# Optimization experiments

Measured on AMD Instinct MI355X. Metric: run time of the kernel, lower is better.

The kernel has to match this reference:

```python
import jax, jax.numpy as jnp
import numpy as np

H = W = M = 16          # 3D token grid
N = H * W * M           # 4096 tokens
D = 256                 # dims == out_dim == key/value dim == x1_dim
HC = 8                  # head_count
D2 = 2 * D              # concat width
C2 = 4 * D              # MixFFN hidden
OUT = D                 # out_dim
UP = OUT // 2           # PatchExpand output channels
B = 4


def _ln(x, g, b, eps=1e-5):
    m = jnp.mean(x, axis=-1, keepdims=True)
    v = jnp.mean(jnp.square(x - m), axis=-1, keepdims=True)
    return (x - m) / jnp.sqrt(v + eps) * g + b


def setup_inputs() -> dict:
    key = jax.random.key(0)
    ks = jax.random.split(key, 16)
    s = 0.02
    inp = {
        "x1": jax.random.normal(ks[0], (B, N, D), jnp.float32),
        "x2": jax.random.normal(ks[1], (B, N, D), jnp.float32),
        # x1_linear (x1_dim -> out_dim)
        "w_x1": s * jax.random.normal(ks[2], (D, OUT), jnp.float32),
        "b_x1": jnp.zeros((OUT,), jnp.float32),
        # CrossAttentionBlock.norm1 (shared for x1 and x2)
        "g_n1": jnp.ones((D,), jnp.float32),
        "be_n1": jnp.zeros((D,), jnp.float32),
        # Cross_Attention.reprojection: 1x1x1 Conv3d D -> 2D == channel matmul
        "w_rep": s * jax.random.normal(ks[3], (D, D2), jnp.float32),
        "b_rep": jnp.zeros((D2,), jnp.float32),
        # Cross_Attention.norm (LayerNorm 2D)
        "g_an": jnp.ones((D2,), jnp.float32),
        "be_an": jnp.zeros((D2,), jnp.float32),
        # CrossAttentionBlock.norm2 (LayerNorm 2D)
        "g_n2": jnp.ones((D2,), jnp.float32),
        "be_n2": jnp.zeros((D2,), jnp.float32),
        # MixFFN_skip fc1 (2D -> 4D), depthwise conv3d, norm1, fc2
        "w_fc1": s * jax.random.normal(ks[4], (D2, C2), jnp.float32),
        "b_fc1": jnp.zeros((C2,), jnp.float32),
        "w_dw": s * jax.random.normal(ks[5], (C2, 1, 3, 3, 3), jnp.float32),
        "b_dw": jnp.zeros((C2,), jnp.float32),
        "g_m1": jnp.ones((C2,), jnp.float32),
        "be_m1": jnp.zeros((C2,), jnp.float32),
        "w_fc2": s * jax.random.normal(ks[6], (C2, D2), jnp.float32),
        "b_fc2": jnp.zeros((D2,), jnp.float32),
        # concat_linear (2*dims -> out_dim)
        "w_cat": s * jax.random.normal(ks[7], (D2, OUT), jnp.float32),
        "b_cat": jnp.zeros((OUT,), jnp.float32),
        # PatchExpand: expand (out_dim -> 4*out_dim, no bias) + LayerNorm(out_dim//2)
        "w_exp": s * jax.random.normal(ks[8], (OUT, 4 * OUT), jnp.float32),
        "g_up": jnp.ones((UP,), jnp.float32),
        "be_up": jnp.zeros((UP,), jnp.float32),
    }
    return inp


def reference(x1, x2, w_x1, b_x1, g_n1, be_n1, w_rep, b_rep, g_an, be_an,
              g_n2, be_n2, w_fc1, b_fc1, w_dw, b_dw, g_m1, be_m1,
              w_fc2, b_fc2, w_cat, b_cat, w_exp, g_up, be_up):
    b = x1.shape[0]
    hk = D // HC  # head key channels (== head value channels here)

    # x1_linear
    x1e = x1 @ w_x1 + b_x1                                 # [B,N,D]

    # shared norm1 applied to both streams
    n1 = _ln(x1e, g_n1, be_n1)
    n2 = _ln(x2, g_n1, be_n1)

    # Cross_Attention (efficient attention, softmax-normalized K/Q)
    kq = jnp.transpose(n2, (0, 2, 1)).reshape(b, HC, hk, N)   # keys==queries
    val = jnp.transpose(n1, (0, 2, 1)).reshape(b, HC, hk, N)
    k = jax.nn.softmax(kq, axis=3)          # softmax over tokens
    q = jax.nn.softmax(kq, axis=2)          # softmax over head channels
    ctx = jnp.einsum('bhkn,bhvn->bhkv', k, val)        # [B,HC,hk,hv]
    att = jnp.einsum('bhkv,bhkn->bhvn', ctx, q)        # [B,HC,hv,N]
    att = att.reshape(b, D, N)                          # concat heads
    # 1x1x1 Conv3d reprojection D -> 2D, then to [B,N,2D] + LayerNorm
    rep = jnp.einsum('bdn,de->bne', att, w_rep) + b_rep
    rep = _ln(rep, g_an, be_an)                         # [B,N,2D]

    # residual concat + attention
    tx = jnp.concatenate([x1e, x2], axis=2) + rep       # [B,N,2D]

    # MixFFN_skip
    h = _ln(tx, g_n2, be_n2) @ w_fc1 + b_fc1            # [B,N,C2]
    hv = jnp.transpose(h, (0, 2, 1)).reshape(b, C2, H, W, M)
    dw = jax.lax.conv_general_dilated(
        hv, w_dw, window_strides=(1, 1, 1), padding='SAME',
        feature_group_count=C2,
        dimension_numbers=('NCDHW', 'OIDHW', 'NCDHW'))
    dw = dw + b_dw[None, :, None, None, None]
    dw = jnp.transpose(dw.reshape(b, C2, N), (0, 2, 1))  # [B,N,C2]
    ax = jax.nn.gelu(_ln(dw + h, g_m1, be_m1), approximate=False)
    mx = tx + (ax @ w_fc2 + b_fc2)                       # [B,N,2D]

    # concat_linear
    y = mx @ w_cat + b_cat                               # [B,N,OUT]

    ye = y @ w_exp                                       # [B,N,4*OUT]
    ye = ye.reshape(b, 8 * N, UP)                        # view+reshape of contiguous
    out = _ln(ye, g_up, be_up)                           # [B,8N,OUT//2]
    return out
```

## Files before the change

### kernel.cpp

```cpp
#include <hip/hip_runtime.h>
#include <math.h>

using u16 = unsigned short;
typedef __bf16 bf16x8 __attribute__((ext_vector_type(8)));
typedef _Float16 h16x8 __attribute__((ext_vector_type(8)));
typedef _Float16 h2 __attribute__((ext_vector_type(2)));
typedef float f32x4 __attribute__((ext_vector_type(4)));

#define BB 4
#define NN 4096
#define DD 256
#define DD2 512
#define CC2 1024
static constexpr int ROWS = BB * NN;
static constexpr size_t MB = 1024 * 1024;

__device__ __forceinline__ u16 f2bf(float f) {
  union { float f; unsigned u; } v; v.f = f;
  unsigned r = v.u + 0x7fffu + ((v.u >> 16) & 1u);
  return (u16)(r >> 16);
}
__device__ __forceinline__ float bf2f(u16 u) {
  union { unsigned u; float f; } v; v.u = ((unsigned)u) << 16;
  return v.f;
}
__device__ __forceinline__ u16 f2h(float f) {
  union { _Float16 h; u16 u; } v; v.h = (_Float16)f; return v.u;
}
__device__ __forceinline__ void gload16(const void* g, void* l) {
  __builtin_amdgcn_global_load_lds(
      (const __attribute__((address_space(1))) void*)g,
      (__attribute__((address_space(3))) void*)l, 16, 0, 0);
}

__global__ __launch_bounds__(256) void wprep_all(
    const float* __restrict__ w_x1, const float* __restrict__ w_rep,
    const float* __restrict__ w_fc1, const float* __restrict__ w_fc2,
    const float* __restrict__ w_cat, const float* __restrict__ w_exp,
    const float* __restrict__ w_dw,
    u16* __restrict__ w_x1t, u16* __restrict__ w_rept,
    u16* __restrict__ w_fc1t, u16* __restrict__ w_fc2h,
    u16* __restrict__ w_catt, u16* __restrict__ w_expt,
    unsigned* __restrict__ w_dwh) {
  int i = blockIdx.x * 256 + threadIdx.x;
  if (i < 65536) { int n = i >> 8, k = i & 255; w_x1t[i] = f2bf(w_x1[k * 256 + n]); return; }
  i -= 65536;
  if (i < 131072) { int n = i >> 8, k = i & 255; w_rept[i] = f2bf(w_rep[k * 512 + n]); return; }
  i -= 131072;
  if (i < 524288) { int n = i >> 9, k = i & 511; w_fc1t[i] = f2bf(w_fc1[k * 1024 + n]); return; }
  i -= 524288;
  if (i < 524288) { int n = i >> 10, k = i & 1023; w_fc2h[i] = f2h(w_fc2[k * 512 + n]); return; }
  i -= 524288;
  if (i < 131072) { int n = i >> 9, k = i & 511; w_catt[i] = f2bf(w_cat[k * 256 + n]); return; }
  i -= 131072;
  if (i < 262144) { int n = i >> 8, k = i & 255; w_expt[i] = f2bf(w_exp[k * 1024 + n]); return; }
  i -= 262144;
  if (i < 13824) {
    int tap = i >> 9, cp = i & 511;
    unsigned lo = f2h(w_dw[(2 * cp) * 27 + tap]);
    unsigned hi = f2h(w_dw[(2 * cp + 1) * 27 + tap]);
    w_dwh[i] = lo | (hi << 16);
  }
}

template <int K, int EPI, bool AF32 = false, bool PERB = false, bool F16 = false>
__global__ __launch_bounds__(256, 2) void gemm_mfma(
    const u16* __restrict__ A, const u16* __restrict__ Bt,
    const float* __restrict__ bias, const u16* __restrict__ resid,
    void* __restrict__ Cout, int nTilesN,
    const float* __restrict__ gup, const float* __restrict__ beup) {
  const int t = threadIdx.x;
  const int bid = blockIdx.x;
  const int m0 = (bid / nTilesN) * 128;
  const int n0 = (bid % nTilesN) * 128;
  const int Ncols = nTilesN * 128;
  if (PERB) Bt += (size_t)(m0 >> 12) * (size_t)Ncols * K;
  const int lane = t & 63, wid = t >> 6;
  const int wr = wid >> 1, wc = wid & 1;
  const int lrow = lane & 15, kgrp = lane >> 4;

  __shared__ u16 ldsA[2][128 * 32];
  __shared__ u16 ldsB[2][128 * 32];

  int srow[2], sslot[2];
#pragma unroll
  for (int c = 0; c < 2; ++c) {
    int idx = c * 256 + t;
    srow[c] = idx >> 2;
    sslot[c] = (idx & 3) ^ ((srow[c] >> 1) & 3);
  }

  int offA[4], offB[4];
#pragma unroll
  for (int m = 0; m < 4; ++m) {
    int r = wr * 64 + m * 16 + lrow;
    offA[m] = r * 32 + ((kgrp ^ ((r >> 1) & 3)) * 8);
  }
#pragma unroll
  for (int n = 0; n < 4; ++n) {
    int r = wc * 64 + n * 16 + lrow;
    offB[n] = r * 32 + ((kgrp ^ ((r >> 1) & 3)) * 8);
  }

  f32x4 acc[4][4];
#pragma unroll
  for (int m = 0; m < 4; ++m)
#pragma unroll
    for (int n = 0; n < 4; ++n) acc[m][n] = f32x4{0.f, 0.f, 0.f, 0.f};

  auto loadA32 = [&](int c, int kc) -> uint4 {
    const float* A32 = (const float*)A;
    const float* p = A32 + (size_t)(m0 + srow[c]) * K + kc + sslot[c] * 8;
    float4 f0 = *(const float4*)p;
    float4 f1 = *(const float4*)(p + 4);
    u16 o[8] = {f2bf(f0.x), f2bf(f0.y), f2bf(f0.z), f2bf(f0.w),
                f2bf(f1.x), f2bf(f1.y), f2bf(f1.z), f2bf(f1.w)};
    return *(uint4*)o;
  };
  auto stage_async = [&](int buf, int kc) {
#pragma unroll
    for (int c = 0; c < 2; ++c) {
      gload16(A + (size_t)(m0 + srow[c]) * K + kc + sslot[c] * 8,
              &ldsA[buf][(c * 256 + t) * 8]);
      gload16(Bt + (size_t)(n0 + srow[c]) * K + kc + sslot[c] * 8,
              &ldsB[buf][(c * 256 + t) * 8]);
    }
  };

  uint4 ra[2], rb[2];
  if constexpr (AF32) {
#pragma unroll
    for (int c = 0; c < 2; ++c) {
      ra[c] = loadA32(c, 0);
      rb[c] = *(const uint4*)(Bt + (size_t)(n0 + srow[c]) * K + sslot[c] * 8);
    }
#pragma unroll
    for (int c = 0; c < 2; ++c) {
      int idx = c * 256 + t;
      *(uint4*)&ldsA[0][idx * 8] = ra[c];
      *(uint4*)&ldsB[0][idx * 8] = rb[c];
    }
  } else {
    stage_async(0, 0);
  }
  __syncthreads();

  const int nt = K / 32;
  for (int tt = 0; tt < nt; ++tt) {
    const int cur = tt & 1;
    if (tt + 1 < nt) {
      const int kc = (tt + 1) * 32;
      if constexpr (AF32) {
#pragma unroll
        for (int c = 0; c < 2; ++c) {
          ra[c] = loadA32(c, kc);
          rb[c] = *(const uint4*)(Bt + (size_t)(n0 + srow[c]) * K + kc + sslot[c] * 8);
        }
      } else {
        stage_async(cur ^ 1, kc);
      }
    }
    if constexpr (F16) {
      h16x8 af[4], bf[4];
#pragma unroll
      for (int m = 0; m < 4; ++m) af[m] = *(const h16x8*)&ldsA[cur][offA[m]];
#pragma unroll
      for (int n = 0; n < 4; ++n) bf[n] = *(const h16x8*)&ldsB[cur][offB[n]];
#pragma unroll
      for (int m = 0; m < 4; ++m)
#pragma unroll
        for (int n = 0; n < 4; ++n)
          acc[m][n] = __builtin_amdgcn_mfma_f32_16x16x32_f16(af[m], bf[n], acc[m][n], 0, 0, 0);
    } else {
      bf16x8 af[4], bf[4];
#pragma unroll
      for (int m = 0; m < 4; ++m) af[m] = *(const bf16x8*)&ldsA[cur][offA[m]];
#pragma unroll
      for (int n = 0; n < 4; ++n) bf[n] = *(const bf16x8*)&ldsB[cur][offB[n]];
#pragma unroll
      for (int m = 0; m < 4; ++m)
#pragma unroll
        for (int n = 0; n < 4; ++n)
          acc[m][n] = __builtin_amdgcn_mfma_f32_16x16x32_bf16(af[m], bf[n], acc[m][n], 0, 0, 0);
    }
    if (AF32 && tt + 1 < nt) {
#pragma unroll
      for (int c = 0; c < 2; ++c) {
        int idx = c * 256 + t;
        *(uint4*)&ldsA[cur ^ 1][idx * 8] = ra[c];
        *(uint4*)&ldsB[cur ^ 1][idx * 8] = rb[c];
      }
    }
    __syncthreads();
  }

  if (EPI == 3) {
    __shared__ float lnS[2][128], lnQ[2][128];
    float s_[4][4], q_[4][4];
#pragma unroll
    for (int m = 0; m < 4; ++m)
#pragma unroll
      for (int j = 0; j < 4; ++j) {
        float s = 0.f, q = 0.f;
#pragma unroll
        for (int n = 0; n < 4; ++n) {
          float v = acc[m][n][j];
          s += v; q += v * v;
        }
        s_[m][j] = s; q_[m][j] = q;
      }
#pragma unroll
    for (int msk = 1; msk < 16; msk <<= 1) {
#pragma unroll
      for (int m = 0; m < 4; ++m)
#pragma unroll
        for (int j = 0; j < 4; ++j) {
          s_[m][j] += __shfl_xor(s_[m][j], msk, 64);
          q_[m][j] += __shfl_xor(q_[m][j], msk, 64);
        }
    }
    if (lrow == 0) {
#pragma unroll
      for (int m = 0; m < 4; ++m)
#pragma unroll
        for (int j = 0; j < 4; ++j) {
          int r = wr * 64 + m * 16 + kgrp * 4 + j;
          lnS[wc][r] = s_[m][j];
          lnQ[wc][r] = q_[m][j];
        }
    }
    __syncthreads();
#pragma unroll
    for (int m = 0; m < 4; ++m) {
      const int rb0 = wr * 64 + m * 16 + kgrp * 4;
#pragma unroll
      for (int j = 0; j < 4; ++j) {
        const int r = rb0 + j;
        float S = lnS[0][r] + lnS[1][r];
        float Q = lnQ[0][r] + lnQ[1][r];
        float mean = S * (1.0f / 128.0f);
        float var = Q * (1.0f / 128.0f) - mean * mean;
        float iv = rsqrtf(var + 1e-5f);
#pragma unroll
        for (int n = 0; n < 4; ++n) {
          int lc = wc * 64 + n * 16 + lrow;
          ((float*)Cout)[(size_t)(m0 + r) * Ncols + n0 + lc] =
              (acc[m][n][j] - mean) * iv * gup[lc] + beup[lc];
        }
      }
    }
    return;
  }

  float bcol[4];
#pragma unroll
  for (int n = 0; n < 4; ++n) {
    int col = n0 + wc * 64 + n * 16 + (lane & 15);
    bcol[n] = bias ? bias[col] : 0.f;
  }
#pragma unroll
  for (int m = 0; m < 4; ++m) {
    const int r0 = m0 + wr * 64 + m * 16 + kgrp * 4;
#pragma unroll
    for (int n = 0; n < 4; ++n) {
      const int col = n0 + wc * 64 + n * 16 + (lane & 15);
#pragma unroll
      for (int j = 0; j < 4; ++j) {
        float v = acc[m][n][j] + bcol[n];
        size_t idx = (size_t)(r0 + j) * Ncols + col;
        if (EPI == 0) {
          ((float*)Cout)[idx] = v;
        } else if (EPI == 1) {
          ((u16*)Cout)[idx] = f2bf(v);
        } else if (EPI == 4) {
          ((u16*)Cout)[idx] = f2h(v);
        } else {
          v += bf2f(resid[idx]);
          ((u16*)Cout)[idx] = f2bf(v);
        }
      }
    }
  }
}

__global__ __launch_bounds__(256) void ln256_both(
    const u16* __restrict__ x1e_b, const float* __restrict__ x2,
    const float* __restrict__ g, const float* __restrict__ be,
    u16* __restrict__ n1T, u16* __restrict__ n2T, u16* __restrict__ qmat) {
  int row = blockIdx.x;
  const int t = threadIdx.x;
  const bool first = row < ROWS;
  if (!first) row -= ROWS;
  __shared__ float ws[8];
  float v = first ? bf2f(x1e_b[(size_t)row * DD + t])
                  : x2[(size_t)row * DD + t];
  float s = v, q = v * v;
#pragma unroll
  for (int m = 1; m < 64; m <<= 1) {
    s += __shfl_xor(s, m, 64);
    q += __shfl_xor(q, m, 64);
  }
  if ((t & 63) == 0) { ws[t >> 6] = s; ws[4 + (t >> 6)] = q; }
  __syncthreads();
  s = ws[0] + ws[1] + ws[2] + ws[3];
  q = ws[4] + ws[5] + ws[6] + ws[7];
  float mean = s * (1.0f / DD);
  float var = q * (1.0f / DD) - mean * mean;
  float iv = rsqrtf(var + 1e-5f);
  u16 rb = f2bf((v - mean) * iv * g[t] + be[t]);
  int b = row >> 12, n = row & 4095;
  if (first) {
    n1T[((size_t)(b * 256 + t)) * 4096 + n] = rb;
  } else {
    n2T[((size_t)(b * 256 + t)) * 4096 + n] = rb;
    float vq = bf2f(rb);
    float hm = vq;
#pragma unroll
    for (int m = 1; m < 32; m <<= 1) hm = fmaxf(hm, __shfl_xor(hm, m, 32));
    float he = __expf(vq - hm);
    float hs = he;
#pragma unroll
    for (int m = 1; m < 32; m <<= 1) hs += __shfl_xor(hs, m, 32);
    qmat[(size_t)row * DD + t] = f2bf(he / hs);
  }
}

__global__ __launch_bounds__(256) void k34_ctx(
    const u16* __restrict__ n2T, const u16* __restrict__ n1T,
    float* __restrict__ ctx) {
  const int bid = blockIdx.x;
  const int bx = (bid & 7) * 128 + (bid >> 3);
  const int b = bx >> 8, d = bx & 255;
  const int h = d >> 5, kk = d & 31;
  const int t = threadIdx.x;
  __shared__ u16 prow[4096];
  __shared__ float xred[8];
  __shared__ float sw[128];
  const u16* src = n2T + (size_t)bx * 4096;
  ((uint4*)prow)[t] = ((const uint4*)src)[t];
  ((uint4*)prow)[256 + t] = ((const uint4*)src)[256 + t];
  __syncthreads();
  float mx = -1e30f;
#pragma unroll
  for (int i = 0; i < 16; ++i) mx = fmaxf(mx, bf2f(prow[i * 256 + t]));
#pragma unroll
  for (int m = 1; m < 64; m <<= 1) mx = fmaxf(mx, __shfl_xor(mx, m, 64));
  if ((t & 63) == 0) xred[t >> 6] = mx;
  __syncthreads();
  mx = fmaxf(fmaxf(xred[0], xred[1]), fmaxf(xred[2], xred[3]));
  float sme = 0.f;
#pragma unroll
  for (int i = 0; i < 16; ++i) sme += __expf(bf2f(prow[i * 256 + t]) - mx);
#pragma unroll
  for (int m = 1; m < 64; m <<= 1) sme += __shfl_xor(sme, m, 64);
  if ((t & 63) == 0) xred[4 + (t >> 6)] = sme;
  __syncthreads();
  const float inv = 1.0f / (xred[4] + xred[5] + xred[6] + xred[7]);

  float acc[32];
#pragma unroll
  for (int v = 0; v < 32; ++v) acc[v] = 0.f;
  const u16* vbase = n1T + ((size_t)(b * 256 + h * 32)) * 4096;
  for (int i = 0; i < 16; ++i) {
    const int n = i * 256 + t;
    const float p = __expf(bf2f(prow[n]) - mx) * inv;
#pragma unroll
    for (int v = 0; v < 32; ++v)
      acc[v] += p * bf2f(vbase[(size_t)v * 4096 + n]);
  }
#pragma unroll
  for (int v = 0; v < 32; ++v) {
#pragma unroll
    for (int m = 1; m < 64; m <<= 1) acc[v] += __shfl_xor(acc[v], m, 64);
  }
  if ((t & 63) == 0) {
#pragma unroll
    for (int v = 0; v < 32; ++v) sw[(t >> 6) * 32 + v] = acc[v];
  }
  __syncthreads();
  if (t < 32)
    ctx[(((size_t)(b * 8 + h)) * 32 + kk) * 32 + t] =
        sw[t] + sw[32 + t] + sw[64 + t] + sw[96 + t];
}

__global__ __launch_bounds__(256) void m2_build(
    const float* __restrict__ ctx, const u16* __restrict__ w_rept,
    u16* __restrict__ m2t) {
  const int b = blockIdx.x >> 4, ec = blockIdx.x & 15;
  const int t = threadIdx.x;
  const int e = ec * 32 + (t >> 3), h = t & 7;
  __shared__ float cl[8192];
#pragma unroll
  for (int i = 0; i < 8; ++i)
    *(float4*)(cl + t * 32 + i * 4) = *(const float4*)(ctx + b * 8192 + t * 32 + i * 4);
  __syncthreads();
  float wf[32];
  {
    u16 wv[32];
#pragma unroll
    for (int i = 0; i < 4; ++i)
      *(uint4*)(wv + i * 8) = *(const uint4*)(w_rept + (size_t)e * 256 + h * 32 + i * 8);
#pragma unroll
    for (int v = 0; v < 32; ++v) wf[v] = bf2f(wv[v]);
  }
  u16 outv[32];
#pragma unroll
  for (int kk = 0; kk < 32; ++kk) {
    float acc = 0.f;
    const float* cp = cl + h * 1024 + kk * 32;
#pragma unroll
    for (int v = 0; v < 32; ++v) acc += cp[v] * wf[v];
    outv[kk] = f2bf(acc);
  }
  u16* dst = m2t + ((size_t)(b * 512 + e)) * 256 + h * 32;
#pragma unroll
  for (int i = 0; i < 4; ++i) *(uint4*)(dst + i * 8) = *(uint4*)(outv + i * 8);
}

__global__ __launch_bounds__(256) void l3_reptx(
    const u16* __restrict__ rep_b, const u16* __restrict__ x1e,
    const float* __restrict__ x2,
    const float* __restrict__ g_an, const float* __restrict__ be_an,
    const float* __restrict__ g_n2, const float* __restrict__ be_n2,
    u16* __restrict__ tx, u16* __restrict__ txln) {
  const int row = blockIdx.x, t = threadIdx.x;
  __shared__ float ws[8];
  float a0 = bf2f(rep_b[(size_t)row * DD2 + t]);
  float a1 = bf2f(rep_b[(size_t)row * DD2 + 256 + t]);
  float s = a0 + a1, q = a0 * a0 + a1 * a1;
#pragma unroll
  for (int m = 1; m < 64; m <<= 1) {
    s += __shfl_xor(s, m, 64);
    q += __shfl_xor(q, m, 64);
  }
  if ((t & 63) == 0) { ws[t >> 6] = s; ws[4 + (t >> 6)] = q; }
  __syncthreads();
  s = ws[0] + ws[1] + ws[2] + ws[3];
  q = ws[4] + ws[5] + ws[6] + ws[7];
  float mean = s * (1.0f / DD2);
  float var = q * (1.0f / DD2) - mean * mean;
  float iv = rsqrtf(var + 1e-5f);
  float r0 = (a0 - mean) * iv * g_an[t] + be_an[t];
  float r1 = (a1 - mean) * iv * g_an[256 + t] + be_an[256 + t];
  float t0 = bf2f(x1e[(size_t)row * DD + t]) + r0;
  float t1 = x2[(size_t)row * DD + t] + r1;
  tx[(size_t)row * DD2 + t] = f2bf(t0);
  tx[(size_t)row * DD2 + 256 + t] = f2bf(t1);
  __syncthreads();
  s = t0 + t1; q = t0 * t0 + t1 * t1;
#pragma unroll
  for (int m = 1; m < 64; m <<= 1) {
    s += __shfl_xor(s, m, 64);
    q += __shfl_xor(q, m, 64);
  }
  if ((t & 63) == 0) { ws[t >> 6] = s; ws[4 + (t >> 6)] = q; }
  __syncthreads();
  s = ws[0] + ws[1] + ws[2] + ws[3];
  q = ws[4] + ws[5] + ws[6] + ws[7];
  mean = s * (1.0f / DD2);
  var = q * (1.0f / DD2) - mean * mean;
  iv = rsqrtf(var + 1e-5f);
  txln[(size_t)row * DD2 + t] = f2bf((t0 - mean) * iv * g_n2[t] + be_n2[t]);
  txln[(size_t)row * DD2 + 256 + t] = f2bf((t1 - mean) * iv * g_n2[256 + t] + be_n2[256 + t]);
}

__global__ __launch_bounds__(512) void c8a_col(
    const u16* __restrict__ h, const unsigned* __restrict__ w_dwh,
    const float* __restrict__ b_dw, const float* __restrict__ g,
    const float* __restrict__ be, u16* __restrict__ ax) {
  const int bid = blockIdx.x;
  const int cidx = (bid & 7) * 128 + (bid >> 3);
  const int b = cidx >> 8, y = (cidx >> 4) & 15, x = cidx & 15;
  const int t = threadIdx.x;
  const int c0 = t * 2;
  const int lane = t & 63, wave = t >> 6;
  const size_t hb = (size_t)b * NN * CC2;

  __shared__ float2 red[16][8];
  __shared__ float2 stats[16];

  int coln[9];
  float cmask[9];
#pragma unroll
  for (int dy = -1; dy <= 1; ++dy)
#pragma unroll
    for (int dx = -1; dx <= 1; ++dx) {
      int qq = (dy + 1) * 3 + (dx + 1);
      int yy = y + dy, xx = x + dx;
      bool ok = ((unsigned)yy < 16u) && ((unsigned)xx < 16u);
      coln[qq] = ((ok ? yy : y) << 4) | (ok ? xx : x);
      cmask[qq] = ok ? 1.f : 0.f;
    }

  h2 wr[3][9];
#pragma unroll
  for (int p = 0; p < 3; ++p)
#pragma unroll
    for (int qq = 0; qq < 9; ++qq) {
      union { unsigned u; h2 h; } w;
      w.u = w_dwh[(p * 9 + qq) * 512 + t];
      _Float16 m = (_Float16)cmask[qq];
      wr[p][qq] = w.h * (h2){m, m};
    }
  h2 bias2 = {(_Float16)b_dw[c0], (_Float16)b_dw[c0 + 1]};

  union { unsigned u; h2 h; } win[3][9];
#define LOADPLANE(ZL, SLOT)                                                   \
  do {                                                                        \
    if ((ZL) >= 0 && (ZL) < 16) {                                             \
      _Pragma("unroll") for (int qq = 0; qq < 9; ++qq) win[SLOT][qq].u =      \
          *(const unsigned*)(h + hb + (size_t)((((ZL) << 8) | coln[qq])) * CC2 + c0); \
    } else {                                                                  \
      _Pragma("unroll") for (int qq = 0; qq < 9; ++qq) win[SLOT][qq].u = 0u;  \
    }                                                                         \
  } while (0)

  LOADPLANE(-1, 0);
  LOADPLANE(0, 1);
  LOADPLANE(1, 2);

  unsigned vs[16];
#pragma unroll
  for (int z = 0; z < 16; ++z) {
    const int pm1 = z % 3, pz = (z + 1) % 3, pp1 = (z + 2) % 3;
    h2 acc = bias2;
#pragma unroll
    for (int qq = 0; qq < 9; ++qq) {
      acc = win[pm1][qq].h * wr[0][qq] + acc;
      acc = win[pz][qq].h * wr[1][qq] + acc;
      acc = win[pp1][qq].h * wr[2][qq] + acc;
    }
    acc = acc + win[pz][4].h;
    LOADPLANE(z + 2, pm1);
    union { h2 h; unsigned u; } pk; pk.h = acc;
    vs[z] = pk.u;
    float v0 = (float)acc[0], v1 = (float)acc[1];
    float s = v0 + v1, q2 = v0 * v0 + v1 * v1;
#pragma unroll
    for (int m = 1; m < 64; m <<= 1) {
      s += __shfl_xor(s, m, 64);
      q2 += __shfl_xor(q2, m, 64);
    }
    if (lane == 0) red[z][wave] = make_float2(s, q2);
  }
#undef LOADPLANE
  __syncthreads();

  for (int zz = wave; zz < 16; zz += 8) {
    float S = (lane < 8) ? red[zz][lane].x : 0.f;
    float Q = (lane < 8) ? red[zz][lane].y : 0.f;
#pragma unroll
    for (int m = 1; m < 8; m <<= 1) {
      S += __shfl_xor(S, m, 64);
      Q += __shfl_xor(Q, m, 64);
    }
    if (lane == 0) {
      float mean = S * (1.0f / CC2);
      float var = Q * (1.0f / CC2) - mean * mean;
      stats[zz] = make_float2(mean, rsqrtf(var + 1e-5f));
    }
  }
  __syncthreads();

  const float g0 = g[c0], g1 = g[c0 + 1], b0 = be[c0], b1 = be[c0 + 1];
#pragma unroll
  for (int z = 0; z < 16; ++z) {
    float2 st = stats[z];
    union { unsigned u; h2 h; } pv; pv.u = vs[z];
    float u0 = ((float)pv.h[0] - st.x) * st.y * g0 + b0;
    float u1 = ((float)pv.h[1] - st.x) * st.y * g1 + b1;
    float s0 = 1.5957691216f * (u0 + 0.044715f * u0 * u0 * u0);
    float s1 = 1.5957691216f * (u1 + 0.044715f * u1 * u1 * u1);
    float o0 = u0 / (1.0f + __expf(-s0));
    float o1 = u1 / (1.0f + __expf(-s1));
    unsigned pk = (unsigned)f2h(o0) | ((unsigned)f2h(o1) << 16);
    *(unsigned*)(ax + ((size_t)(b * NN + ((z << 8) | (y << 4) | x))) * CC2 + c0) = pk;
  }
}

extern "C" void kernel_launch(void* const* d_in, const int* in_sizes, int n_in,
                              void* d_out, int out_size, void* d_ws, size_t ws_size,
                              hipStream_t stream) {
  const float* x1    = (const float*)d_in[0];
  const float* x2    = (const float*)d_in[1];
  const float* w_x1  = (const float*)d_in[2];
  const float* b_x1  = (const float*)d_in[3];
  const float* g_n1  = (const float*)d_in[4];
  const float* be_n1 = (const float*)d_in[5];
  const float* w_rep = (const float*)d_in[6];
  const float* b_rep = (const float*)d_in[7];
  const float* g_an  = (const float*)d_in[8];
  const float* be_an = (const float*)d_in[9];
  const float* g_n2  = (const float*)d_in[10];
  const float* be_n2 = (const float*)d_in[11];
  const float* w_fc1 = (const float*)d_in[12];
  const float* b_fc1 = (const float*)d_in[13];
  const float* w_dw  = (const float*)d_in[14];
  const float* b_dw  = (const float*)d_in[15];
  const float* g_m1  = (const float*)d_in[16];
  const float* be_m1 = (const float*)d_in[17];
  const float* w_fc2 = (const float*)d_in[18];
  const float* b_fc2 = (const float*)d_in[19];
  const float* w_cat = (const float*)d_in[20];
  const float* b_cat = (const float*)d_in[21];
  const float* w_exp = (const float*)d_in[22];
  const float* g_up  = (const float*)d_in[23];
  const float* be_up = (const float*)d_in[24];

  char* ws = (char*)d_ws;
  float* out = (float*)d_out;

  u16*   qmat    = (u16*)(ws + 0);
  u16*   x1e_b   = (u16*)(ws + 8 * MB);
  u16*   n1T     = (u16*)(ws + 24 * MB);
  u16*   n2T     = (u16*)(ws + 40 * MB);
  float* ctx     = (float*)(ws + 48 * MB);
  u16*   rep_b   = (u16*)(ws + 49 * MB);
  u16*   tx      = (u16*)(ws + 81 * MB);
  u16*   txln    = (u16*)(ws + 97 * MB);
  u16*   hbuf    = (u16*)(ws + 113 * MB);
  u16*   ax      = (u16*)(ws + 49 * MB);
  u16*   mx      = (u16*)(ws + 8 * MB);
  u16*   ybuf    = (u16*)(ws + 0);
  u16*   w_x1t   = (u16*)(ws + 145 * MB);
  u16*   w_rept  = w_x1t + 256 * 256;
  u16*   w_fc1t  = w_rept + 512 * 256;
  u16*   w_fc2h  = w_fc1t + 1024 * 512;
  u16*   w_catt  = w_fc2h + 512 * 1024;
  u16*   w_expt  = w_catt + 256 * 512;
  unsigned* w_dwh = (unsigned*)(ws + 149 * MB);
  u16*   m2t     = (u16*)(ws + 152 * MB);

  wprep_all<<<(1652224 + 255) / 256, 256, 0, stream>>>(
      w_x1, w_rep, w_fc1, w_fc2, w_cat, w_exp, w_dw,
      w_x1t, w_rept, w_fc1t, w_fc2h, w_catt, w_expt, w_dwh);

  gemm_mfma<256, 1, true><<<(ROWS / 128) * 2, 256, 0, stream>>>(
      (const u16*)x1, w_x1t, b_x1, nullptr, x1e_b, 2, nullptr, nullptr);
  ln256_both<<<2 * ROWS, 256, 0, stream>>>(x1e_b, x2, g_n1, be_n1, n1T, n2T, qmat);
  k34_ctx<<<BB * 256, 256, 0, stream>>>(n2T, n1T, ctx);
  m2_build<<<64, 256, 0, stream>>>(ctx, w_rept, m2t);
  gemm_mfma<256, 1, false, true><<<(ROWS / 128) * 4, 256, 0, stream>>>(
      qmat, m2t, b_rep, nullptr, rep_b, 4, nullptr, nullptr);
  l3_reptx<<<ROWS, 256, 0, stream>>>(rep_b, x1e_b, x2, g_an, be_an, g_n2, be_n2, tx, txln);
  gemm_mfma<512, 4><<<(ROWS / 128) * 8, 256, 0, stream>>>(
      txln, w_fc1t, b_fc1, nullptr, hbuf, 8, nullptr, nullptr);
  c8a_col<<<1024, 512, 0, stream>>>(hbuf, w_dwh, b_dw, g_m1, be_m1, ax);
  gemm_mfma<1024, 2, false, false, true><<<(ROWS / 128) * 4, 256, 0, stream>>>(
      ax, w_fc2h, b_fc2, tx, mx, 4, nullptr, nullptr);
  gemm_mfma<512, 1><<<(ROWS / 128) * 2, 256, 0, stream>>>(
      mx, w_catt, b_cat, nullptr, ybuf, 2, nullptr, nullptr);
  gemm_mfma<256, 3><<<(ROWS / 128) * 8, 256, 0, stream>>>(
      ybuf, w_expt, nullptr, nullptr, out, 8, g_up, be_up);
}
```

Measured before the change: 300.7 us.

## Tile LayerNorm with shared-memory transpose for coalesced transposed writes and bf16 x2 copy

Replaces the one-row-per-block LayerNorm kernel with a 32-row tile kernel. Each wave normalizes a row with vectorized loads and wave-only reductions, then the tile is transposed through shared memory so the n1T/n2T stores are coalesced 16-byte writes instead of scattered 2-byte strided writes. The kernel also writes a bf16 copy of x2, which the later residual kernel reads instead of the fp32 x2. This cuts global traffic, but the residual path now uses x2 rounded to bf16 and the kernel needs extra shared memory.

```diff
diff --git a/kernel.cpp b/kernel.cpp
--- a/kernel.cpp
+++ b/kernel.cpp
@@ -283,45 +283,83 @@
   }
 }
 
-__global__ __launch_bounds__(256) void ln256_both(
+__global__ __launch_bounds__(256) void ln_tr(
     const u16* __restrict__ x1e_b, const float* __restrict__ x2,
     const float* __restrict__ g, const float* __restrict__ be,
-    u16* __restrict__ n1T, u16* __restrict__ n2T, u16* __restrict__ qmat) {
-  int row = blockIdx.x;
+    u16* __restrict__ n1T, u16* __restrict__ n2T,
+    u16* __restrict__ x2b, u16* __restrict__ qmat) {
+  int bid = blockIdx.x;
+  const bool first = bid < 512;
+  if (!first) bid -= 512;
+  const int r0 = bid * 32;
+  const int b = r0 >> 12;
+  const int nloc = r0 & (NN - 1);
   const int t = threadIdx.x;
-  const bool first = row < ROWS;
-  if (!first) row -= ROWS;
-  __shared__ float ws[8];
-  float v = first ? bf2f(x1e_b[(size_t)row * DD + t])
-                  : x2[(size_t)row * DD + t];
-  float s = v, q = v * v;
-#pragma unroll
-  for (int m = 1; m < 64; m <<= 1) {
-    s += __shfl_xor(s, m, 64);
-    q += __shfl_xor(q, m, 64);
-  }
-  if ((t & 63) == 0) { ws[t >> 6] = s; ws[4 + (t >> 6)] = q; }
-  __syncthreads();
-  s = ws[0] + ws[1] + ws[2] + ws[3];
-  q = ws[4] + ws[5] + ws[6] + ws[7];
-  float mean = s * (1.0f / DD);
-  float var = q * (1.0f / DD) - mean * mean;
-  float iv = rsqrtf(var + 1e-5f);
-  u16 rb = f2bf((v - mean) * iv * g[t] + be[t]);
-  int b = row >> 12, n = row & 4095;
-  if (first) {
-    n1T[((size_t)(b * 256 + t)) * 4096 + n] = rb;
-  } else {
-    n2T[((size_t)(b * 256 + t)) * 4096 + n] = rb;
-    float vq = bf2f(rb);
-    float hm = vq;
-#pragma unroll
-    for (int m = 1; m < 32; m <<= 1) hm = fmaxf(hm, __shfl_xor(hm, m, 32));
-    float he = __expf(vq - hm);
-    float hs = he;
-#pragma unroll
-    for (int m = 1; m < 32; m <<= 1) hs += __shfl_xor(hs, m, 32);
-    qmat[(size_t)row * DD + t] = f2bf(he / hs);
+  const int lane = t & 63, wave = t >> 6;
+  const int d0 = lane * 4;
+  __shared__ u16 tile[32][264];
+
+  float gv[4], bv[4];
+#pragma unroll
+  for (int j = 0; j < 4; ++j) { gv[j] = g[d0 + j]; bv[j] = be[d0 + j]; }
+
+#pragma unroll
+  for (int it = 0; it < 8; ++it) {
+    const int row = r0 + it * 4 + wave;
+    float v[4];
+    if (first) {
+      uint2 u = *(const uint2*)(x1e_b + (size_t)row * DD + d0);
+      v[0] = bf2f((u16)(u.x & 0xffff)); v[1] = bf2f((u16)(u.x >> 16));
+      v[2] = bf2f((u16)(u.y & 0xffff)); v[3] = bf2f((u16)(u.y >> 16));
+    } else {
+      float4 f = *(const float4*)(x2 + (size_t)row * DD + d0);
+      v[0] = f.x; v[1] = f.y; v[2] = f.z; v[3] = f.w;
+      u16 raw[4] = {f2bf(f.x), f2bf(f.y), f2bf(f.z), f2bf(f.w)};
+      *(uint2*)(x2b + (size_t)row * DD + d0) = *(uint2*)raw;
+    }
+    float s = v[0] + v[1] + v[2] + v[3];
+    float q = v[0] * v[0] + v[1] * v[1] + v[2] * v[2] + v[3] * v[3];
+#pragma unroll
+    for (int m = 1; m < 64; m <<= 1) {
+      s += __shfl_xor(s, m, 64);
+      q += __shfl_xor(q, m, 64);
+    }
+    float mean = s * (1.0f / DD);
+    float var = q * (1.0f / DD) - mean * mean;
+    float iv = rsqrtf(var + 1e-5f);
+    const int rit = it * 4 + wave;
+    u16 o[4];
+#pragma unroll
+    for (int j = 0; j < 4; ++j) o[j] = f2bf((v[j] - mean) * iv * gv[j] + bv[j]);
+    *(uint2*)&tile[rit][d0] = *(uint2*)o;
+    if (!first) {
+      float lb[4] = {bf2f(o[0]), bf2f(o[1]), bf2f(o[2]), bf2f(o[3])};
+      float hm = fmaxf(fmaxf(lb[0], lb[1]), fmaxf(lb[2], lb[3]));
+#pragma unroll
+      for (int m = 1; m < 8; m <<= 1) hm = fmaxf(hm, __shfl_xor(hm, m, 64));
+      float he[4], hs = 0.f;
+#pragma unroll
+      for (int j = 0; j < 4; ++j) { he[j] = __expf(lb[j] - hm); hs += he[j]; }
+#pragma unroll
+      for (int m = 1; m < 8; m <<= 1) hs += __shfl_xor(hs, m, 64);
+      float inv = 1.0f / hs;
+      u16 qo[4];
+#pragma unroll
+      for (int j = 0; j < 4; ++j) qo[j] = f2bf(he[j] * inv);
+      *(uint2*)(qmat + (size_t)row * DD + d0) = *(uint2*)qo;
+    }
+  }
+  __syncthreads();
+
+  u16* dstT = first ? n1T : n2T;
+#pragma unroll
+  for (int i = 0; i < 4; ++i) {
+    int chunk = i * 256 + t;
+    int d = chunk >> 2, nc = chunk & 3;
+    u16 vals[8];
+#pragma unroll
+    for (int k = 0; k < 8; ++k) vals[k] = tile[nc * 8 + k][d];
+    *(uint4*)(dstT + ((size_t)(b * 256 + d)) * 4096 + nloc + nc * 8) = *(uint4*)vals;
   }
 }
 
@@ -419,7 +457,7 @@
 
 __global__ __launch_bounds__(256) void l3_reptx(
     const u16* __restrict__ rep_b, const u16* __restrict__ x1e,
-    const float* __restrict__ x2,
+    const u16* __restrict__ x2b,
     const float* __restrict__ g_an, const float* __restrict__ be_an,
     const float* __restrict__ g_n2, const float* __restrict__ be_n2,
     u16* __restrict__ tx, u16* __restrict__ txln) {
@@ -443,7 +481,7 @@
   float r0 = (a0 - mean) * iv * g_an[t] + be_an[t];
   float r1 = (a1 - mean) * iv * g_an[256 + t] + be_an[256 + t];
   float t0 = bf2f(x1e[(size_t)row * DD + t]) + r0;
-  float t1 = x2[(size_t)row * DD + t] + r1;
+  float t1 = bf2f(x2b[(size_t)row * DD + t]) + r1;
   tx[(size_t)row * DD2 + t] = f2bf(t0);
   tx[(size_t)row * DD2 + 256 + t] = f2bf(t1);
   __syncthreads();
@@ -613,6 +651,7 @@
   u16*   qmat    = (u16*)(ws + 0);
   u16*   x1e_b   = (u16*)(ws + 8 * MB);
   u16*   n1T     = (u16*)(ws + 24 * MB);
+  u16*   x2bb    = (u16*)(ws + 32 * MB);
   u16*   n2T     = (u16*)(ws + 40 * MB);
   float* ctx     = (float*)(ws + 48 * MB);
   u16*   rep_b   = (u16*)(ws + 49 * MB);
@@ -637,12 +676,13 @@
 
   gemm_mfma<256, 1, true><<<(ROWS / 128) * 2, 256, 0, stream>>>(
       (const u16*)x1, w_x1t, b_x1, nullptr, x1e_b, 2, nullptr, nullptr);
-  ln256_both<<<2 * ROWS, 256, 0, stream>>>(x1e_b, x2, g_n1, be_n1, n1T, n2T, qmat);
+  ln_tr<<<1024, 256, 0, stream>>>(x1e_b, x2, g_n1, be_n1, n1T, n2T, x2bb, qmat);
   k34_ctx<<<BB * 256, 256, 0, stream>>>(n2T, n1T, ctx);
   m2_build<<<64, 256, 0, stream>>>(ctx, w_rept, m2t);
   gemm_mfma<256, 1, false, true><<<(ROWS / 128) * 4, 256, 0, stream>>>(
       qmat, m2t, b_rep, nullptr, rep_b, 4, nullptr, nullptr);
-  l3_reptx<<<ROWS, 256, 0, stream>>>(rep_b, x1e_b, x2, g_an, be_an, g_n2, be_n2, tx, txln);
+  l3_reptx<<<ROWS, 256, 0, stream>>>(rep_b, x1e_b, x2bb, g_an, be_an,
+                                     g_n2, be_n2, tx, txln);
   gemm_mfma<512, 4><<<(ROWS / 128) * 8, 256, 0, stream>>>(
       txln, w_fc1t, b_fc1, nullptr, hbuf, 8, nullptr, nullptr);
   c8a_col<<<1024, 512, 0, stream>>>(hbuf, w_dwh, b_dw, g_m1, be_m1, ax);
```

Result: faster. 271.5 us, median of 2 (-9.7%).
